# Kernel tuning notes

Hardware: AMD Instinct MI355X
Metric: run time of the kernel (lower is better)

The kernel has to match this reference:

```python
import jax, jax.numpy as jnp
import numpy as np

N = 8192
IN_FEATURES = 512
OUT_FEATURES = 256
ALPHA = 0.2  # LeakyReLU negative slope
MASK_VAL = -1e11


def setup_inputs() -> dict:
    key = jax.random.key(0)
    k_h, k_adj, k_w, k_a1, k_a2 = jax.random.split(key, 5)
    h = jax.random.normal(k_h, (N, IN_FEATURES), dtype=jnp.float32)
    adj = jax.random.randint(k_adj, (N, N), 0, 2, dtype=jnp.int32)
    # xavier_uniform with gain=1.414 for Linear weight [out, in]
    def xavier(k, fan_out, fan_in, gain=1.414):
        bound = gain * np.sqrt(6.0 / (fan_in + fan_out))
        return jax.random.uniform(k, (fan_out, fan_in), dtype=jnp.float32,
                                  minval=-bound, maxval=bound)
    W = xavier(k_w, OUT_FEATURES, IN_FEATURES)          # linear_w.weight
    a1 = xavier(k_a1, 1, OUT_FEATURES)[0]               # linear_a_1.weight -> [out]
    a2 = xavier(k_a2, 1, OUT_FEATURES)[0]               # linear_a_2.weight -> [out]
    return {"h": h, "W": W, "a1": a1, "a2": a2, "adj": adj}


def reference(h, W, a1, a2, adj):
    # wh: [N, F_out]
    wh = jnp.einsum("ni,oi->no", h, W)
    wh1 = wh @ a1  # [N]
    wh2 = wh @ a2  # [N]
    # additive attention scores e_ij = leakyrelu(wh1_i + wh2_j): [N, N]
    e = jax.nn.leaky_relu(wh1[:, None] + wh2[None, :], negative_slope=ALPHA)
    scores = jnp.where(adj > 0, e, MASK_VAL)
    attention = jax.nn.softmax(scores, axis=-1)  # dropout p=0 -> identity
    h_new = attention @ wh  # [N, F_out]
    return jax.nn.elu(h_new)  # concat=True path
```

## Files before the change

kernel.cpp:

```cpp
#include <hip/hip_runtime.h>


typedef __attribute__((ext_vector_type(8))) short short8;
typedef __attribute__((ext_vector_type(4))) float f32x4;

#define LOG2E 1.4426950408889634f

__device__ __forceinline__ unsigned short f2bf(float f) {
  unsigned int u = __float_as_uint(f);
  unsigned int r = u + 0x7FFFu + ((u >> 16) & 1u);
  return (unsigned short)(r >> 16);
}

__global__ __launch_bounds__(256) void k_mask(const int* __restrict__ adj,
                                              unsigned long long* __restrict__ bm) {
  const int row = blockIdx.x * 4 + (threadIdx.x >> 6);
  const int lane = threadIdx.x & 63;
  const int* ap = adj + (size_t)row * 8192 + lane;
  unsigned long long* bp = bm + (size_t)row * 128;
#pragma unroll 2
  for (int c = 0; c < 128; c += 4) {
    int v0 = ap[(c + 0) * 64];
    int v1 = ap[(c + 1) * 64];
    int v2 = ap[(c + 2) * 64];
    int v3 = ap[(c + 3) * 64];
    unsigned long long m0 = __ballot(v0 > 0);
    unsigned long long m1 = __ballot(v1 > 0);
    unsigned long long m2 = __ballot(v2 > 0);
    unsigned long long m3 = __ballot(v3 > 0);
    if (lane == 0) {
      *(ulonglong2*)(bp + c) = make_ulonglong2(m0, m1);
      *(ulonglong2*)(bp + c + 2) = make_ulonglong2(m2, m3);
    }
  }
}

__global__ __launch_bounds__(512) void k_u(const float* __restrict__ W,
                                           const float* __restrict__ a1,
                                           const float* __restrict__ a2,
                                           float* __restrict__ u1,
                                           float* __restrict__ u2) {
  __shared__ float p1[16][32], p2[16][32];
  const int tid = threadIdx.x;
  const int kk = tid & 31, og = tid >> 5;
  const int k0 = blockIdx.x * 32;
  float s1 = 0.f, s2 = 0.f;
#pragma unroll
  for (int j = 0; j < 16; j++) {
    const int o = og * 16 + j;
    const float w = W[(size_t)o * 512 + k0 + kk];
    s1 += w * a1[o];
    s2 += w * a2[o];
  }
  p1[og][kk] = s1;
  p2[og][kk] = s2;
  __syncthreads();
  if (tid < 32) {
    float t1 = 0.f, t2 = 0.f;
#pragma unroll
    for (int g = 0; g < 16; g++) { t1 += p1[g][tid]; t2 += p2[g][tid]; }
    u1[k0 + tid] = t1;
    u2[k0 + tid] = t2;
  }
}

__global__ __launch_bounds__(256) void k_rowvec(const float* __restrict__ h,
                                                const float* __restrict__ u1,
                                                const float* __restrict__ u2,
                                                float* __restrict__ wh1,
                                                float* __restrict__ wh2,
                                                float* __restrict__ pmax) {
  __shared__ float su1[512], su2[512];
  __shared__ float smax[4];
  const int tid = threadIdx.x;
  for (int i = tid; i < 512; i += 256) { su1[i] = u1[i]; su2[i] = u2[i]; }
  __syncthreads();
  const int lane = tid & 63;
  const int row = blockIdx.x * 4 + (tid >> 6);
  const float* hp = h + (size_t)row * 512 + lane * 8;
  float4 x0 = *(const float4*)hp;
  float4 x1 = *(const float4*)(hp + 4);
  const float* q1 = su1 + lane * 8;
  const float* q2 = su2 + lane * 8;
  float s1 = x0.x * q1[0] + x0.y * q1[1] + x0.z * q1[2] + x0.w * q1[3]
           + x1.x * q1[4] + x1.y * q1[5] + x1.z * q1[6] + x1.w * q1[7];
  float s2 = x0.x * q2[0] + x0.y * q2[1] + x0.z * q2[2] + x0.w * q2[3]
           + x1.x * q2[4] + x1.y * q2[5] + x1.z * q2[6] + x1.w * q2[7];
#pragma unroll
  for (int off = 32; off >= 1; off >>= 1) {
    s1 += __shfl_xor(s1, off);
    s2 += __shfl_xor(s2, off);
  }
  if (lane == 0) {
    wh1[row] = s1 * LOG2E;
    wh2[row] = s2 * LOG2E;
    smax[tid >> 6] = s2 * LOG2E;
  }
  __syncthreads();
  if (tid == 0)
    pmax[blockIdx.x] = fmaxf(fmaxf(smax[0], smax[1]), fmaxf(smax[2], smax[3]));
}

__global__ __launch_bounds__(512, 1) void k_wh(const float* __restrict__ h,
                                               const float* __restrict__ W,
                                               unsigned short* __restrict__ whT,
                                               const float* __restrict__ pmax,
                                               float* __restrict__ gmax) {
  __shared__ uint4 lds[2560];
  __shared__ float sred[8];
  const int tid = threadIdx.x;
  if (blockIdx.x == 0) {
    float m = -3.0e38f;
    for (int i = tid; i < 2048; i += 512) m = fmaxf(m, pmax[i]);
#pragma unroll
    for (int off = 32; off >= 1; off >>= 1) m = fmaxf(m, __shfl_xor(m, off));
    if ((tid & 63) == 0) sred[tid >> 6] = m;
    __syncthreads();
    if (tid == 0) {
      float g = sred[0];
#pragma unroll
      for (int i = 1; i < 8; i++) g = fmaxf(g, sred[i]);
      gmax[0] = g;
    }
  }
  const int i0 = blockIdx.x * 64;
  const int lane = tid & 63, wid = tid >> 6;
  const int wm = wid >> 2, wn = wid & 3;
  const int l16 = lane & 15, lq = lane >> 4;
  const int hr = tid >> 3, hc = tid & 7;
  const int wr = tid >> 1, wc = tid & 1;

  f32x4 acc[2][4] = {};

  for (int t = 0; t < 8; t++) {
    const int k0 = t * 64;
    const float* hp = h + (size_t)(i0 + hr) * 512 + k0 + hc * 8;
    float4 hx = *(const float4*)hp;
    float4 hy = *(const float4*)(hp + 4);
    const float* wp = W + (size_t)wr * 512 + k0 + wc * 32;
    float4 wv[8];
#pragma unroll
    for (int q = 0; q < 8; q++) wv[q] = *(const float4*)(wp + q * 4);

    __syncthreads();
    uint4 hw;
    hw.x = (unsigned)f2bf(hx.x) | ((unsigned)f2bf(hx.y) << 16);
    hw.y = (unsigned)f2bf(hx.z) | ((unsigned)f2bf(hx.w) << 16);
    hw.z = (unsigned)f2bf(hy.x) | ((unsigned)f2bf(hy.y) << 16);
    hw.w = (unsigned)f2bf(hy.z) | ((unsigned)f2bf(hy.w) << 16);
    lds[hr * 8 + (hc ^ (hr & 7))] = hw;
#pragma unroll
    for (int q = 0; q < 4; q++) {
      uint4 ww;
      ww.x = (unsigned)f2bf(wv[2 * q].x) | ((unsigned)f2bf(wv[2 * q].y) << 16);
      ww.y = (unsigned)f2bf(wv[2 * q].z) | ((unsigned)f2bf(wv[2 * q].w) << 16);
      ww.z = (unsigned)f2bf(wv[2 * q + 1].x) | ((unsigned)f2bf(wv[2 * q + 1].y) << 16);
      ww.w = (unsigned)f2bf(wv[2 * q + 1].z) | ((unsigned)f2bf(wv[2 * q + 1].w) << 16);
      lds[512 + wr * 8 + ((wc * 4 + q) ^ (wr & 7))] = ww;
    }
    __syncthreads();
#pragma unroll
    for (int ks = 0; ks < 2; ks++) {
      const int r0 = wm * 32 + l16, r1 = r0 + 16;
      short8 fa0 = *(const short8*)&lds[r0 * 8 + ((ks * 4 + lq) ^ (r0 & 7))];
      short8 fa1 = *(const short8*)&lds[r1 * 8 + ((ks * 4 + lq) ^ (r1 & 7))];
#pragma unroll
      for (int fn = 0; fn < 4; fn++) {
        const int bn = wn * 64 + fn * 16 + l16;
        short8 fb = *(const short8*)&lds[512 + bn * 8 + ((ks * 4 + lq) ^ (bn & 7))];
        acc[0][fn] = __builtin_amdgcn_mfma_f32_16x16x32_bf16(fa0, fb, acc[0][fn], 0, 0, 0);
        acc[1][fn] = __builtin_amdgcn_mfma_f32_16x16x32_bf16(fa1, fb, acc[1][fn], 0, 0, 0);
      }
    }
  }
#pragma unroll
  for (int fm = 0; fm < 2; fm++) {
#pragma unroll
    for (int fn = 0; fn < 4; fn++) {
      const int n = wn * 64 + fn * 16 + l16;
      const int m0 = i0 + wm * 32 + fm * 16 + lq * 4;
      uint2 o;
      o.x = (unsigned)f2bf(acc[fm][fn][0]) | ((unsigned)f2bf(acc[fm][fn][1]) << 16);
      o.y = (unsigned)f2bf(acc[fm][fn][2]) | ((unsigned)f2bf(acc[fm][fn][3]) << 16);
      *(uint2*)(whT + (size_t)n * 8192 + m0) = o;
    }
  }
}

struct PFR {
  unsigned long long lo, hi;
};

__global__ __launch_bounds__(512, 1) void k_attn(
    const unsigned long long* __restrict__ bm, const unsigned short* __restrict__ whT,
    const float* __restrict__ wh1v, const float* __restrict__ wh2v,
    const float* __restrict__ gmax,
    float* __restrict__ out0, float* __restrict__ out1,
    float* __restrict__ out2, float* __restrict__ out3,
    float* __restrict__ denp) {
  __shared__ uint4 ring[2][2048];
  __shared__ float wh2s[2048];
  const int NT = 32;
  const int tid = threadIdx.x;
  const int bid = blockIdx.x;
  const int sb = (bid & 7) >> 1;
  const int mb = ((bid >> 3) << 1) | (bid & 1);
  const int i0 = mb * 128;
  const int jbase = sb * 2048;
  const int lane = tid & 63, wid = tid >> 6;
  const int wm = wid >> 1, wn = wid & 1;
  const int l16 = lane & 15, q = lane >> 4;
  const int row_lo = i0 + wm * 32 + l16;

  if (tid < 512) ((float4*)wh2s)[tid] = ((const float4*)(wh2v + jbase))[tid];

  const float M2 = gmax[0];
  const float w1lo = wh1v[row_lo];
  const float w1hi = wh1v[row_lo + 16];
  float tv = w1lo + M2;
  const float Milo = tv > 0.f ? tv : 0.2f * tv;
  tv = w1hi + M2;
  const float Mihi = tv > 0.f ? tv : 0.2f * tv;
  const float c1lo = w1lo - Milo, c2lo = 0.2f * w1lo - Milo;
  const float c1hi = w1hi - Mihi, c2hi = 0.2f * w1hi - Mihi;

  const unsigned long long* bmp_lo = bm + (size_t)row_lo * 128 + sb * 32;
  const unsigned long long* bmp_hi = bmp_lo + 16 * 128;

  f32x4 accL[8] = {}, accH[8] = {};
  float dsL = 0.f, dsH = 0.f;
  short8 paL0, paL1, paH0, paH1;
  PFR PA, PB;

#define PFLOAD(R, T)                              \
  do {                                            \
    const int t_ = ((T) < NT) ? (T) : 0;          \
    R.lo = bmp_lo[t_];                            \
    R.hi = bmp_hi[t_];                            \
  } while (0)

#define COMPUTE(R, T)                                                          \
  do {                                                                         \
    const int o_ = (((T) < NT) ? (T) : 0) * 64 + q * 8;                        \
    float4 z0 = *(const float4*)(wh2s + o_);                                   \
    float4 z1 = *(const float4*)(wh2s + o_ + 4);                               \
    float4 z2 = *(const float4*)(wh2s + o_ + 32);                              \
    float4 z3 = *(const float4*)(wh2s + o_ + 36);                              \
    float zv[16] = {z0.x, z0.y, z0.z, z0.w, z1.x, z1.y, z1.z, z1.w,            \
                    z2.x, z2.y, z2.z, z2.w, z3.x, z3.y, z3.z, z3.w};           \
    const unsigned msl[2] = {(unsigned)(R.lo >> (q * 8)),                      \
                             (unsigned)(R.lo >> (32 + q * 8))};                \
    const unsigned msh[2] = {(unsigned)(R.hi >> (q * 8)),                      \
                             (unsigned)(R.hi >> (32 + q * 8))};                \
    float pl[16], ph[16];                                                      \
    _Pragma("unroll") for (int i = 0; i < 16; i++) {                           \
      float e1 = fmaxf(c1lo + zv[i], __builtin_fmaf(0.2f, zv[i], c2lo));       \
      float p = (msl[i >> 3] & (1u << (i & 7))) ? __builtin_amdgcn_exp2f(e1)   \
                                                : 0.f;                         \
      pl[i] = p;                                                               \
      dsL += p;                                                                \
      float e2 = fmaxf(c1hi + zv[i], __builtin_fmaf(0.2f, zv[i], c2hi));       \
      p = (msh[i >> 3] & (1u << (i & 7))) ? __builtin_amdgcn_exp2f(e2) : 0.f;  \
      ph[i] = p;                                                               \
      dsH += p;                                                                \
    }                                                                          \
    _Pragma("unroll") for (int i = 0; i < 8; i++) {                            \
      paL0[i] = (short)f2bf(pl[i]);                                            \
      paL1[i] = (short)f2bf(pl[8 + i]);                                        \
      paH0[i] = (short)f2bf(ph[i]);                                            \
      paH1[i] = (short)f2bf(ph[8 + i]);                                        \
    }                                                                          \
  } while (0)

#define STAGE(TT, SLOT)                                                        \
  do {                                                                         \
    const int tt_ = ((TT) < NT) ? (TT) : 0;                                    \
    const size_t gj_ = (size_t)(jbase + tt_ * 64);                             \
    _Pragma("unroll") for (int kq = 0; kq < 4; kq++) {                         \
      const int L = kq * 512 + tid;                                            \
      const int row = L >> 3, sub = L & 7;                                     \
      const int boff = (sub * 16) ^ ((row & 7) << 4);                          \
      const char* src_ = (const char*)(whT + (size_t)row * 8192 + gj_) + boff; \
      char* dst_ = (char*)ring[SLOT] + L * 16;                                 \
      __builtin_amdgcn_global_load_lds(                                        \
          (const __attribute__((address_space(1))) unsigned int*)src_,         \
          (__attribute__((address_space(3))) unsigned int*)dst_, 16, 0, 0);    \
    }                                                                          \
  } while (0)

#define FENCE asm volatile("s_waitcnt vmcnt(2)" ::: "memory")

#define MFMAPH(SLOT)                                                           \
  do {                                                                         \
    const char* lb_ = (const char*)ring[SLOT];                                 \
    _Pragma("unroll") for (int nb = 0; nb < 8; nb++) {                         \
      const int n_ = wn * 128 + nb * 16 + l16;                                 \
      const int rb_ = n_ * 128;                                                \
      const int sw_ = (n_ & 7) << 4;                                           \
      short8 fb0 = *(const short8*)(lb_ + rb_ + ((q * 16) ^ sw_));             \
      short8 fb1 = *(const short8*)(lb_ + rb_ + ((64 + q * 16) ^ sw_));        \
      accL[nb] = __builtin_amdgcn_mfma_f32_16x16x32_bf16(paL0, fb0, accL[nb], 0, 0, 0); \
      accL[nb] = __builtin_amdgcn_mfma_f32_16x16x32_bf16(paL1, fb1, accL[nb], 0, 0, 0); \
      accH[nb] = __builtin_amdgcn_mfma_f32_16x16x32_bf16(paH0, fb0, accH[nb], 0, 0, 0); \
      accH[nb] = __builtin_amdgcn_mfma_f32_16x16x32_bf16(paH1, fb1, accH[nb], 0, 0, 0); \
    }                                                                          \
  } while (0)

  PFLOAD(PA, 0);
  STAGE(0, 0);
  __syncthreads();

  for (int t = 0; t < NT; t += 2) {
    PFLOAD(PB, t + 1);
    COMPUTE(PA, t);
    FENCE;
    __builtin_amdgcn_s_barrier();
    STAGE(t + 1, 1);
    MFMAPH(0);
    PFLOAD(PA, t + 2);
    COMPUTE(PB, t + 1);
    FENCE;
    __builtin_amdgcn_s_barrier();
    STAGE(t + 2, 0);
    MFMAPH(1);
  }

#undef PFLOAD
#undef COMPUTE
#undef STAGE
#undef FENCE
#undef MFMAPH

  float* outp = (sb == 0) ? out0 : (sb == 1) ? out1 : (sb == 2) ? out2 : out3;
  const int r0 = i0 + wm * 32 + q * 4;
#pragma unroll
  for (int nb = 0; nb < 8; nb++) {
    const int col = wn * 128 + nb * 16 + l16;
#pragma unroll
    for (int r = 0; r < 4; r++) {
      outp[(size_t)(r0 + r) * 256 + col] = accL[nb][r];
      outp[(size_t)(r0 + 16 + r) * 256 + col] = accH[nb][r];
    }
  }

  dsL += __shfl_xor(dsL, 16);
  dsL += __shfl_xor(dsL, 32);
  dsH += __shfl_xor(dsH, 16);
  dsH += __shfl_xor(dsH, 32);
  if (wn == 0 && lane < 16) {
    denp[sb * 8192 + i0 + wm * 32 + lane] = dsL;
    denp[sb * 8192 + i0 + wm * 32 + 16 + lane] = dsH;
  }
}

__global__ __launch_bounds__(256) void k_out(float* __restrict__ out,
                                             const float* __restrict__ p1,
                                             const float* __restrict__ p2,
                                             const float* __restrict__ p3,
                                             const float* __restrict__ denp) {
  const int idx = blockIdx.x * 256 + threadIdx.x;
  const int row = idx >> 6;
  float4 o = ((const float4*)out)[idx];
  float4 a = ((const float4*)p1)[idx];
  float4 b = ((const float4*)p2)[idx];
  float4 c = ((const float4*)p3)[idx];
  const float inv =
      1.0f / (denp[row] + denp[8192 + row] + denp[16384 + row] + denp[24576 + row]);
  float v0 = (o.x + a.x + b.x + c.x) * inv;
  float v1 = (o.y + a.y + b.y + c.y) * inv;
  float v2 = (o.z + a.z + b.z + c.z) * inv;
  float v3 = (o.w + a.w + b.w + c.w) * inv;
  v0 = v0 > 0.f ? v0 : expm1f(v0);
  v1 = v1 > 0.f ? v1 : expm1f(v1);
  v2 = v2 > 0.f ? v2 : expm1f(v2);
  v3 = v3 > 0.f ? v3 : expm1f(v3);
  ((float4*)out)[idx] = make_float4(v0, v1, v2, v3);
}

extern "C" void kernel_launch(void* const* d_in, const int* in_sizes, int n_in,
                              void* d_out, int out_size, void* d_ws, size_t ws_size,
                              hipStream_t stream) {
  const float* h = (const float*)d_in[0];
  const float* W = (const float*)d_in[1];
  const float* a1 = (const float*)d_in[2];
  const float* a2 = (const float*)d_in[3];
  const int* adj = (const int*)d_in[4];
  float* out = (float*)d_out;
  char* ws = (char*)d_ws;

  unsigned short* whT = (unsigned short*)ws;
  float* part1 = (float*)(ws + (4u << 20));
  float* part2 = (float*)(ws + (12u << 20));
  float* part3 = (float*)(ws + (20u << 20));
  float* denp = (float*)(ws + (28u << 20));
  float* wh1 = denp + 4 * 8192;
  float* wh2 = wh1 + 8192;
  float* pmax = wh2 + 8192;
  float* u1 = pmax + 2048;
  float* u2 = u1 + 512;
  float* gmax = u2 + 512;
  unsigned long long* bm = (unsigned long long*)(ws + (29u << 20));

  hipLaunchKernelGGL(k_mask, dim3(2048), dim3(256), 0, stream, adj, bm);
  hipLaunchKernelGGL(k_u, dim3(16), dim3(512), 0, stream, W, a1, a2, u1, u2);
  hipLaunchKernelGGL(k_rowvec, dim3(2048), dim3(256), 0, stream, h, u1, u2, wh1,
                     wh2, pmax);
  hipLaunchKernelGGL(k_wh, dim3(128), dim3(512), 0, stream, h, W, whT, pmax, gmax);
  hipLaunchKernelGGL(k_attn, dim3(256), dim3(512), 0, stream, bm, whT, wh1,
                     wh2, gmax, out, part1, part2, part3, denp);
  hipLaunchKernelGGL(k_out, dim3(2048), dim3(256), 0, stream, out, part1, part2,
                     part3, denp);
  (void)in_sizes; (void)n_in; (void)out_size; (void)ws_size;
}
```

Baseline: 176.2 us.

## Split attention over eight column slices and coalesce mask loads via column permutation

The attention kernel now splits the j dimension into 8 slices instead of 4, launching 512 blocks with a launch-bounds occupancy hint of 4. This is meant to fill more CUs and overlap more work. The mask kernel reads adjacency as int4 vectors, and a matching column permutation (jperm) is applied to wh2 and to the whT stores so bit positions stay consistent. In exchange, more partial outputs must be written and reduced in k_out, which adds memory traffic. The whT stores also become scalar 16-bit writes.

```diff
diff --git a/kernel.cpp b/kernel.cpp
--- a/kernel.cpp
+++ b/kernel.cpp
@@ -12,25 +12,26 @@
   return (unsigned short)(r >> 16);
 }
 
+__device__ __forceinline__ int jperm(int j) {
+  return (j & ~255) | ((j & 3) << 6) | ((j >> 2) & 63);
+}
+
 __global__ __launch_bounds__(256) void k_mask(const int* __restrict__ adj,
                                               unsigned long long* __restrict__ bm) {
   const int row = blockIdx.x * 4 + (threadIdx.x >> 6);
   const int lane = threadIdx.x & 63;
-  const int* ap = adj + (size_t)row * 8192 + lane;
+  const int* ap = adj + (size_t)row * 8192 + lane * 4;
   unsigned long long* bp = bm + (size_t)row * 128;
-#pragma unroll 2
-  for (int c = 0; c < 128; c += 4) {
-    int v0 = ap[(c + 0) * 64];
-    int v1 = ap[(c + 1) * 64];
-    int v2 = ap[(c + 2) * 64];
-    int v3 = ap[(c + 3) * 64];
-    unsigned long long m0 = __ballot(v0 > 0);
-    unsigned long long m1 = __ballot(v1 > 0);
-    unsigned long long m2 = __ballot(v2 > 0);
-    unsigned long long m3 = __ballot(v3 > 0);
+#pragma unroll 4
+  for (int T = 0; T < 32; T++) {
+    int4 v = *(const int4*)(ap + T * 256);
+    unsigned long long m0 = __ballot(v.x > 0);
+    unsigned long long m1 = __ballot(v.y > 0);
+    unsigned long long m2 = __ballot(v.z > 0);
+    unsigned long long m3 = __ballot(v.w > 0);
     if (lane == 0) {
-      *(ulonglong2*)(bp + c) = make_ulonglong2(m0, m1);
-      *(ulonglong2*)(bp + c + 2) = make_ulonglong2(m2, m3);
+      *(ulonglong2*)(bp + T * 4) = make_ulonglong2(m0, m1);
+      *(ulonglong2*)(bp + T * 4 + 2) = make_ulonglong2(m2, m3);
     }
   }
 }
@@ -93,7 +94,7 @@
   }
   if (lane == 0) {
     wh1[row] = s1 * LOG2E;
-    wh2[row] = s2 * LOG2E;
+    wh2[jperm(row)] = s2 * LOG2E;
     smax[tid >> 6] = s2 * LOG2E;
   }
   __syncthreads();
@@ -179,40 +180,35 @@
     for (int fn = 0; fn < 4; fn++) {
       const int n = wn * 64 + fn * 16 + l16;
       const int m0 = i0 + wm * 32 + fm * 16 + lq * 4;
-      uint2 o;
-      o.x = (unsigned)f2bf(acc[fm][fn][0]) | ((unsigned)f2bf(acc[fm][fn][1]) << 16);
-      o.y = (unsigned)f2bf(acc[fm][fn][2]) | ((unsigned)f2bf(acc[fm][fn][3]) << 16);
-      *(uint2*)(whT + (size_t)n * 8192 + m0) = o;
-    }
-  }
-}
-
-struct PFR {
-  unsigned long long lo, hi;
-};
-
-__global__ __launch_bounds__(512, 1) void k_attn(
+      const int base = (m0 & ~255) | ((m0 >> 2) & 63);
+#pragma unroll
+      for (int r = 0; r < 4; r++)
+        whT[(size_t)n * 8192 + (base | (r << 6))] = f2bf(acc[fm][fn][r]);
+    }
+  }
+}
+
+__global__ __launch_bounds__(512, 4) void k_attn(
     const unsigned long long* __restrict__ bm, const unsigned short* __restrict__ whT,
     const float* __restrict__ wh1v, const float* __restrict__ wh2v,
     const float* __restrict__ gmax,
-    float* __restrict__ out0, float* __restrict__ out1,
-    float* __restrict__ out2, float* __restrict__ out3,
+    float* __restrict__ out0, float* __restrict__ parts,
     float* __restrict__ denp) {
   __shared__ uint4 ring[2][2048];
-  __shared__ float wh2s[2048];
-  const int NT = 32;
+  __shared__ float wh2s[1024];
+  const int NT = 16;
   const int tid = threadIdx.x;
   const int bid = blockIdx.x;
-  const int sb = (bid & 7) >> 1;
-  const int mb = ((bid >> 3) << 1) | (bid & 1);
+  const int sb = bid & 7;
+  const int mb = bid >> 3;
   const int i0 = mb * 128;
-  const int jbase = sb * 2048;
+  const int jbase = sb * 1024;
   const int lane = tid & 63, wid = tid >> 6;
   const int wm = wid >> 1, wn = wid & 1;
   const int l16 = lane & 15, q = lane >> 4;
   const int row_lo = i0 + wm * 32 + l16;
 
-  if (tid < 512) ((float4*)wh2s)[tid] = ((const float4*)(wh2v + jbase))[tid];
+  if (tid < 256) ((float4*)wh2s)[tid] = ((const float4*)(wh2v + jbase))[tid];
 
   const float M2 = gmax[0];
   const float w1lo = wh1v[row_lo];
@@ -224,22 +220,22 @@
   const float c1lo = w1lo - Milo, c2lo = 0.2f * w1lo - Milo;
   const float c1hi = w1hi - Mihi, c2hi = 0.2f * w1hi - Mihi;
 
-  const unsigned long long* bmp_lo = bm + (size_t)row_lo * 128 + sb * 32;
+  const unsigned long long* bmp_lo = bm + (size_t)row_lo * 128 + sb * 16;
   const unsigned long long* bmp_hi = bmp_lo + 16 * 128;
 
   f32x4 accL[8] = {}, accH[8] = {};
   float dsL = 0.f, dsH = 0.f;
   short8 paL0, paL1, paH0, paH1;
-  PFR PA, PB;
-
-#define PFLOAD(R, T)                              \
+  unsigned long long PAlo, PAhi, PBlo, PBhi;
+
+#define PFLOAD(Rlo, Rhi, T)                       \
   do {                                            \
     const int t_ = ((T) < NT) ? (T) : 0;          \
-    R.lo = bmp_lo[t_];                            \
-    R.hi = bmp_hi[t_];                            \
+    Rlo = bmp_lo[t_];                             \
+    Rhi = bmp_hi[t_];                             \
   } while (0)
 
-#define COMPUTE(R, T)                                                          \
+#define COMPUTE(Rlo, Rhi, T)                                                   \
   do {                                                                         \
     const int o_ = (((T) < NT) ? (T) : 0) * 64 + q * 8;                        \
     float4 z0 = *(const float4*)(wh2s + o_);                                   \
@@ -248,27 +244,37 @@
     float4 z3 = *(const float4*)(wh2s + o_ + 36);                              \
     float zv[16] = {z0.x, z0.y, z0.z, z0.w, z1.x, z1.y, z1.z, z1.w,            \
                     z2.x, z2.y, z2.z, z2.w, z3.x, z3.y, z3.z, z3.w};           \
-    const unsigned msl[2] = {(unsigned)(R.lo >> (q * 8)),                      \
-                             (unsigned)(R.lo >> (32 + q * 8))};                \
-    const unsigned msh[2] = {(unsigned)(R.hi >> (q * 8)),                      \
-                             (unsigned)(R.hi >> (32 + q * 8))};                \
-    float pl[16], ph[16];                                                      \
-    _Pragma("unroll") for (int i = 0; i < 16; i++) {                           \
-      float e1 = fmaxf(c1lo + zv[i], __builtin_fmaf(0.2f, zv[i], c2lo));       \
-      float p = (msl[i >> 3] & (1u << (i & 7))) ? __builtin_amdgcn_exp2f(e1)   \
-                                                : 0.f;                         \
-      pl[i] = p;                                                               \
-      dsL += p;                                                                \
-      float e2 = fmaxf(c1hi + zv[i], __builtin_fmaf(0.2f, zv[i], c2hi));       \
-      p = (msh[i >> 3] & (1u << (i & 7))) ? __builtin_amdgcn_exp2f(e2) : 0.f;  \
-      ph[i] = p;                                                               \
-      dsH += p;                                                                \
+    {                                                                          \
+      const unsigned ms0 = (unsigned)(Rlo >> (q * 8));                         \
+      const unsigned ms1 = (unsigned)(Rlo >> (32 + q * 8));                    \
+      float pl[16];                                                            \
+      _Pragma("unroll") for (int i = 0; i < 16; i++) {                         \
+        float e1 = fmaxf(c1lo + zv[i], __builtin_fmaf(0.2f, zv[i], c2lo));     \
+        const unsigned mbit = (i < 8) ? (ms0 >> i) : (ms1 >> (i - 8));         \
+        float p = (mbit & 1u) ? __builtin_amdgcn_exp2f(e1) : 0.f;              \
+        pl[i] = p;                                                             \
+        dsL += p;                                                              \
+      }                                                                        \
+      _Pragma("unroll") for (int i = 0; i < 8; i++) {                          \
+        paL0[i] = (short)f2bf(pl[i]);                                          \
+        paL1[i] = (short)f2bf(pl[8 + i]);                                      \
+      }                                                                        \
     }                                                                          \
-    _Pragma("unroll") for (int i = 0; i < 8; i++) {                            \
-      paL0[i] = (short)f2bf(pl[i]);                                            \
-      paL1[i] = (short)f2bf(pl[8 + i]);                                        \
-      paH0[i] = (short)f2bf(ph[i]);                                            \
-      paH1[i] = (short)f2bf(ph[8 + i]);                                        \
+    {                                                                          \
+      const unsigned ms0 = (unsigned)(Rhi >> (q * 8));                         \
+      const unsigned ms1 = (unsigned)(Rhi >> (32 + q * 8));                    \
+      float ph[16];                                                            \
+      _Pragma("unroll") for (int i = 0; i < 16; i++) {                         \
+        float e2 = fmaxf(c1hi + zv[i], __builtin_fmaf(0.2f, zv[i], c2hi));     \
+        const unsigned mbit = (i < 8) ? (ms0 >> i) : (ms1 >> (i - 8));         \
+        float p = (mbit & 1u) ? __builtin_amdgcn_exp2f(e2) : 0.f;              \
+        ph[i] = p;                                                             \
+        dsH += p;                                                              \
+      }                                                                        \
+      _Pragma("unroll") for (int i = 0; i < 8; i++) {                          \
+        paH0[i] = (short)f2bf(ph[i]);                                          \
+        paH1[i] = (short)f2bf(ph[8 + i]);                                      \
+      }                                                                        \
     }                                                                          \
   } while (0)
 
@@ -306,19 +312,19 @@
     }                                                                          \
   } while (0)
 
-  PFLOAD(PA, 0);
+  PFLOAD(PAlo, PAhi, 0);
   STAGE(0, 0);
   __syncthreads();
 
   for (int t = 0; t < NT; t += 2) {
-    PFLOAD(PB, t + 1);
-    COMPUTE(PA, t);
+    PFLOAD(PBlo, PBhi, t + 1);
+    COMPUTE(PAlo, PAhi, t);
     FENCE;
     __builtin_amdgcn_s_barrier();
     STAGE(t + 1, 1);
     MFMAPH(0);
-    PFLOAD(PA, t + 2);
-    COMPUTE(PB, t + 1);
+    PFLOAD(PAlo, PAhi, t + 2);
+    COMPUTE(PBlo, PBhi, t + 1);
     FENCE;
     __builtin_amdgcn_s_barrier();
     STAGE(t + 2, 0);
@@ -331,7 +337,7 @@
 #undef FENCE
 #undef MFMAPH
 
-  float* outp = (sb == 0) ? out0 : (sb == 1) ? out1 : (sb == 2) ? out2 : out3;
+  float* outp = (sb == 0) ? out0 : parts + (size_t)(sb - 1) * 2097152;
   const int r0 = i0 + wm * 32 + q * 4;
 #pragma unroll
   for (int nb = 0; nb < 8; nb++) {
@@ -354,22 +360,20 @@
 }
 
 __global__ __launch_bounds__(256) void k_out(float* __restrict__ out,
-                                             const float* __restrict__ p1,
-                                             const float* __restrict__ p2,
-                                             const float* __restrict__ p3,
+                                             const float* __restrict__ parts,
                                              const float* __restrict__ denp) {
   const int idx = blockIdx.x * 256 + threadIdx.x;
   const int row = idx >> 6;
   float4 o = ((const float4*)out)[idx];
-  float4 a = ((const float4*)p1)[idx];
-  float4 b = ((const float4*)p2)[idx];
-  float4 c = ((const float4*)p3)[idx];
-  const float inv =
-      1.0f / (denp[row] + denp[8192 + row] + denp[16384 + row] + denp[24576 + row]);
-  float v0 = (o.x + a.x + b.x + c.x) * inv;
-  float v1 = (o.y + a.y + b.y + c.y) * inv;
-  float v2 = (o.z + a.z + b.z + c.z) * inv;
-  float v3 = (o.w + a.w + b.w + c.w) * inv;
+  float den = denp[row];
+#pragma unroll
+  for (int s = 1; s < 8; s++) {
+    float4 p = ((const float4*)(parts + (size_t)(s - 1) * 2097152))[idx];
+    o.x += p.x; o.y += p.y; o.z += p.z; o.w += p.w;
+    den += denp[s * 8192 + row];
+  }
+  const float inv = 1.0f / den;
+  float v0 = o.x * inv, v1 = o.y * inv, v2 = o.z * inv, v3 = o.w * inv;
   v0 = v0 > 0.f ? v0 : expm1f(v0);
   v1 = v1 > 0.f ? v1 : expm1f(v1);
   v2 = v2 > 0.f ? v2 : expm1f(v2);
@@ -389,26 +393,23 @@
   char* ws = (char*)d_ws;
 
   unsigned short* whT = (unsigned short*)ws;
-  float* part1 = (float*)(ws + (4u << 20));
-  float* part2 = (float*)(ws + (12u << 20));
-  float* part3 = (float*)(ws + (20u << 20));
-  float* denp = (float*)(ws + (28u << 20));
-  float* wh1 = denp + 4 * 8192;
+  float* parts = (float*)(ws + (4u << 20));
+  float* denp = (float*)(ws + (60u << 20));
+  float* wh1 = denp + 8 * 8192;
   float* wh2 = wh1 + 8192;
   float* pmax = wh2 + 8192;
   float* u1 = pmax + 2048;
   float* u2 = u1 + 512;
   float* gmax = u2 + 512;
-  unsigned long long* bm = (unsigned long long*)(ws + (29u << 20));
+  unsigned long long* bm = (unsigned long long*)(ws + (61u << 20));
 
   hipLaunchKernelGGL(k_mask, dim3(2048), dim3(256), 0, stream, adj, bm);
   hipLaunchKernelGGL(k_u, dim3(16), dim3(512), 0, stream, W, a1, a2, u1, u2);
   hipLaunchKernelGGL(k_rowvec, dim3(2048), dim3(256), 0, stream, h, u1, u2, wh1,
                      wh2, pmax);
   hipLaunchKernelGGL(k_wh, dim3(128), dim3(512), 0, stream, h, W, whT, pmax, gmax);
-  hipLaunchKernelGGL(k_attn, dim3(256), dim3(512), 0, stream, bm, whT, wh1,
-                     wh2, gmax, out, part1, part2, part3, denp);
-  hipLaunchKernelGGL(k_out, dim3(2048), dim3(256), 0, stream, out, part1, part2,
-                     part3, denp);
+  hipLaunchKernelGGL(k_attn, dim3(512), dim3(512), 0, stream, bm, whT, wh1,
+                     wh2, gmax, out, parts, denp);
+  hipLaunchKernelGGL(k_out, dim3(2048), dim3(256), 0, stream, out, parts, denp);
   (void)in_sizes; (void)n_in; (void)out_size; (void)ws_size;
 }
```

New measurement: 317.2 us. 80.0% more time.
